# Kernel tuning notes

Measured on AMD Instinct MI355X. Metric: run time of the kernel, lower is better.

Reference implementation:

```python
import jax, jax.numpy as jnp
import numpy as np
from jax import lax

N, D, BATCH = 8192, 256, 64


def setup_inputs() -> dict:
    key = jax.random.key(0)
    V = jax.random.normal(key, (N, D), dtype=jnp.float32)
    V = V / jnp.linalg.norm(V, axis=1, keepdims=True)  # cosine = raw dot product
    return {
        "V": V,
        "cos_threshold": jnp.array([0.25], dtype=jnp.float32),
        "batch_size": BATCH,
    }


def reference(V, cos_threshold, batch_size):
    """Faithful port of Embeddings._fast_predict: batched cosine-sim thresholding
    followed by a sequential transitive merge of group ids.

    Returns group_ids [N] int32 (the clustering result; the torch code wraps this
    into a Matcher object, which is pure python bookkeeping).
    """
    n, d = V.shape
    B = int(batch_size)
    n_batches = n // B
    thr = cos_threshold[0]
    j_idx = jnp.arange(n, dtype=jnp.int32)
    group_init = jnp.arange(n, dtype=jnp.int32)

    def outer(gids, batch_start):
        # group ids as of the start of this batch (torch computes batch_matched
        # with these, but reads live group_ids inside the row loop via views)
        g0 = gids
        Vb = lax.dynamic_slice(V, (batch_start, 0), (B, d))        # [B, D]
        sims = Vb @ V.T                                            # [B, N]
        g0_i = lax.dynamic_slice(g0, (batch_start,), (B,))         # [B]
        jmask = j_idx > batch_start                                # j_slice = batch_start+1 .. N
        mask = (sims >= thr) & jmask[None, :] & (g0_i[:, None] != g0[None, :])  # [B, N]

        def inner(g, inp):
            k, row = inp
            gi = g[batch_start + k]  # live group id of row i (torch g_i is a view)
            # isin(group_ids, matched_groups): flag[label]=1 if any matched j has
            # current group label == label, then gather back through g
            flag = jnp.zeros(n, jnp.int32).at[g].max(row.astype(jnp.int32))
            g = jnp.where(flag[g] > 0, gi, g)
            return g, None

        gids, _ = lax.scan(inner, gids, (jnp.arange(B, dtype=jnp.int32), mask))
        return gids, None

    starts = jnp.arange(n_batches, dtype=jnp.int32) * B
    gids, _ = lax.scan(outer, group_init, starts)
    return gids
```

## Files before the change

kernel.cpp:

```cpp
#include <hip/hip_runtime.h>
#include <stdint.h>

#define NPTS 8192
#define DIM  256
#define CAP  32768
#define LDSE 8192
#define IBCAP 256
#define BAND 2.0e-3f

typedef _Float16 f16x8  __attribute__((ext_vector_type(8)));
typedef float    f32x16 __attribute__((ext_vector_type(16)));


__global__ __launch_bounds__(256) void convert_kernel(
        const float* __restrict__ V, _Float16* __restrict__ Vh,
        unsigned* __restrict__ ctr) {
    if (blockIdx.x == 0 && threadIdx.x == 0) { ctr[0] = 0u; ctr[1] = 0u; }
    size_t t = (size_t)blockIdx.x * 256 + threadIdx.x;
    const float4* src = reinterpret_cast<const float4*>(V) + t * 2;
    float4 v0 = src[0], v1 = src[1];
    f16x8 h;
    h[0] = (_Float16)v0.x; h[1] = (_Float16)v0.y;
    h[2] = (_Float16)v0.z; h[3] = (_Float16)v0.w;
    h[4] = (_Float16)v1.x; h[5] = (_Float16)v1.y;
    h[6] = (_Float16)v1.z; h[7] = (_Float16)v1.w;
    *reinterpret_cast<f16x8*>(Vh + t * 8) = h;
}

__global__ void init_count(unsigned* ctr) {
    if (threadIdx.x == 0) { ctr[0] = 0u; ctr[1] = 0u; }
}

__device__ __forceinline__ void gload_lds16(const void* g, void* l) {
    __builtin_amdgcn_global_load_lds(
        (const __attribute__((address_space(1))) void*)g,
        (__attribute__((address_space(3))) void*)l, 16, 0, 0);
}

__global__ __launch_bounds__(256, 2) void edge_mfma(
        const _Float16* __restrict__ Vh,
        const float* __restrict__ V,
        const float* __restrict__ thr_p,
        unsigned* __restrict__ ctr,
        unsigned* __restrict__ edges) {
    int t = blockIdx.x;
    int bi = (int)((65.0f - sqrtf(4225.0f - 4.0f * (float)t)) * 0.5f);
    if (bi > 31) bi = 31;
    while (bi > 0 && bi * (65 - bi) > t) --bi;
    while ((bi + 1) * (64 - bi) <= t) ++bi;
    int bj = 2 * bi + (t - bi * (65 - bi));

    __shared__ _Float16 LA[2][256 * 32];
    __shared__ _Float16 LB[2][128 * 32];
    __shared__ unsigned ibl[IBCAP];
    __shared__ unsigned ibn;

    const float thr = thr_p[0];
    const float hi = thr + BAND, lo = thr - BAND;
    const int tid  = threadIdx.x;
    const int lane = tid & 63;
    const int wid  = tid >> 6;
    const int wr = wid >> 1, wc = wid & 1;
    const int i0 = bi * 256, j0 = bj * 128;

    if (tid == 0) ibn = 0u;

    f32x16 acc[4][2];
#pragma unroll
    for (int a = 0; a < 4; ++a)
#pragma unroll
        for (int b = 0; b < 2; ++b) acc[a][b] = 0.0f;

    const int l31 = lane & 31, g = lane >> 5;
    const int srow = lane >> 2;
    const int sblk = lane & 3;

    auto STAGE = [&](int buf, int kc) {
#pragma unroll
        for (int q = 0; q < 6; ++q) {
            const int qq = wid * 6 + q;
            if (qq < 16) {
                const int grow = i0 + qq * 16 + srow;
                gload_lds16(Vh + ((size_t)grow * DIM + kc + sblk * 8),
                            &LA[buf][qq * 512]);
            } else {
                const int ins = qq - 16;
                const int grow = j0 + ins * 16 + srow;
                gload_lds16(Vh + ((size_t)grow * DIM + kc + sblk * 8),
                            &LB[buf][ins * 512]);
            }
        }
    };

    auto COMPUTE = [&](int buf) {
#pragma unroll
        for (int s = 0; s < 2; ++s) {
            const int xo = s * 16 + g * 8;
            f16x8 af[4], bf[2];
#pragma unroll
            for (int a = 0; a < 4; ++a)
                af[a] = *(const f16x8*)&LA[buf][(wr * 128 + a * 32 + l31) * 32 + xo];
#pragma unroll
            for (int b = 0; b < 2; ++b)
                bf[b] = *(const f16x8*)&LB[buf][(wc * 64 + b * 32 + l31) * 32 + xo];
#pragma unroll
            for (int a = 0; a < 4; ++a)
#pragma unroll
                for (int b = 0; b < 2; ++b)
                    acc[a][b] = __builtin_amdgcn_mfma_f32_32x32x16_f16(
                        af[a], bf[b], acc[a][b], 0, 0, 0);
        }
    };

    STAGE(0, 0);
    __syncthreads();
#pragma unroll
    for (int it = 0; it < 8; ++it) {
        if (it < 7) STAGE((it + 1) & 1, (it + 1) * 32);
        COMPUTE(it & 1);
        __syncthreads();
    }

#pragma unroll
    for (int a = 0; a < 4; ++a)
#pragma unroll
        for (int b = 0; b < 2; ++b)
#pragma unroll
            for (int reg = 0; reg < 16; ++reg) {
                float sim = acc[a][b][reg];
                int rr = (reg & 3) + 8 * (reg >> 2) + 4 * g;
                int i = i0 + wr * 128 + a * 32 + rr;
                int j = j0 + wc * 64 + b * 32 + l31;
                if (j > i && sim >= lo) {
                    unsigned key = ((unsigned)i << 13) | (unsigned)j;
                    if (sim >= hi) {
                        unsigned p = atomicAdd(&ctr[0], 1u);
                        if (p < CAP) edges[p] = key;
                    } else {
                        unsigned p = atomicAdd(&ibn, 1u);
                        if (p < IBCAP) ibl[p] = key;
                    }
                }
            }
    __syncthreads();

    unsigned nib = ibn; if (nib > IBCAP) nib = IBCAP;
    const double thrd = (double)thr;
    for (unsigned q = tid; q < nib; q += 256) {
        unsigned key = ibl[q];
        int i = (int)(key >> 13), j = (int)(key & 8191u);
        const float4* a4 = reinterpret_cast<const float4*>(V + (size_t)i * DIM);
        const float4* b4 = reinterpret_cast<const float4*>(V + (size_t)j * DIM);
        double s = 0.0;
#pragma unroll 4
        for (int k = 0; k < DIM / 4; ++k) {
            float4 x = a4[k], y = b4[k];
            s += (double)x.x * y.x + (double)x.y * y.y
               + (double)x.z * y.z + (double)x.w * y.w;
        }
        if (s >= thrd) {
            unsigned p = atomicAdd(&ctr[0], 1u);
            if (p < CAP) edges[p] = key;
        }
    }
}

__global__ __launch_bounds__(256) void edge_kernel(
        const float* __restrict__ V,
        const float* __restrict__ thr_p,
        unsigned*    __restrict__ ctr,
        unsigned*    __restrict__ edges) {
    const int bi = blockIdx.y, bj = blockIdx.x;
    if (bj < bi) return;

    __shared__ float As[128 * 32];
    __shared__ float Bs[128 * 32];

    const float thr = thr_p[0];
    const int tid = threadIdx.x;
    const int tx = tid & 15, ty = tid >> 4;
    const int i0 = bi * 128, j0 = bj * 128;

    float acc[8][8];
#pragma unroll
    for (int r = 0; r < 8; ++r)
#pragma unroll
        for (int c = 0; c < 8; ++c) acc[r][c] = 0.f;

    const int srow = tid >> 3, sq = tid & 7;

    for (int kc = 0; kc < DIM; kc += 32) {
#pragma unroll
        for (int p = 0; p < 4; ++p) {
            int row = srow + 32 * p;
            float4 va = *reinterpret_cast<const float4*>(
                &V[(size_t)(i0 + row) * DIM + kc + sq * 4]);
            float4 vb = *reinterpret_cast<const float4*>(
                &V[(size_t)(j0 + row) * DIM + kc + sq * 4]);
            int w = row * 32 + ((sq ^ ((row >> 3) & 7)) << 2);
            *reinterpret_cast<float4*>(&As[w]) = va;
            *reinterpret_cast<float4*>(&Bs[w]) = vb;
        }
        __syncthreads();
#pragma unroll
        for (int k4 = 0; k4 < 8; ++k4) {
            const float* pA = &As[(ty * 8) * 32 + ((k4 ^ (ty & 7)) << 2)];
            const float* pB = &Bs[(tx * 8) * 32 + ((k4 ^ (tx & 7)) << 2)];
            float4 a[8], b[8];
#pragma unroll
            for (int r = 0; r < 8; ++r)
                a[r] = *reinterpret_cast<const float4*>(&pA[r * 32]);
#pragma unroll
            for (int c = 0; c < 8; ++c)
                b[c] = *reinterpret_cast<const float4*>(&pB[c * 32]);
#pragma unroll
            for (int r = 0; r < 8; ++r)
#pragma unroll
                for (int c = 0; c < 8; ++c) {
                    acc[r][c] = fmaf(a[r].x, b[c].x, acc[r][c]);
                    acc[r][c] = fmaf(a[r].y, b[c].y, acc[r][c]);
                    acc[r][c] = fmaf(a[r].z, b[c].z, acc[r][c]);
                    acc[r][c] = fmaf(a[r].w, b[c].w, acc[r][c]);
                }
        }
        __syncthreads();
    }
#pragma unroll
    for (int r = 0; r < 8; ++r)
#pragma unroll
        for (int c = 0; c < 8; ++c) {
            int i = i0 + ty * 8 + r;
            int j = j0 + tx * 8 + c;
            if (j > i && acc[r][c] >= thr) {
                unsigned p = atomicAdd(&ctr[0], 1u);
                if (p < CAP) edges[p] = ((unsigned)i << 13) | (unsigned)j;
            }
        }
}

__global__ __launch_bounds__(1024) void uf_kernel(
        const unsigned* __restrict__ ctr,
        const unsigned* __restrict__ edges,
        int* __restrict__ out) {
    __shared__ int      par[NPTS];
    __shared__ unsigned slotA[NPTS];
    __shared__ unsigned slotB[NPTS];
    __shared__ unsigned sedge[LDSE];

    const int tid = threadIdx.x;

    unsigned EC = ctr[0]; if (EC > LDSE) EC = LDSE;

    for (int t = tid; t < NPTS; t += 1024) {
        par[t] = t; slotA[t] = 0xFFFFFFFFu; slotB[t] = 0xFFFFFFFFu;
    }
    for (unsigned e = tid; e < EC; e += 1024) sedge[e] = edges[e];
    __syncthreads();

    volatile int* vpar = par;

    for (int round = 0;; ++round) {
        unsigned* S = (round & 1) ? slotB : slotA;
        unsigned* T = (round & 1) ? slotA : slotB;

        for (unsigned e = tid; e < EC; e += 1024) {
            unsigned key = sedge[e];
            if (key & 0x80000000u) continue;
            int ri = (int)(key >> 13), rj = (int)(key & 8191u);
            int p;
            while ((p = vpar[ri]) != ri) ri = p;
            while ((p = vpar[rj]) != rj) rj = p;
            atomicMin(&S[ri], key);
            atomicMin(&S[rj], key);
        }
        __syncthreads();

        int mylive = 0;
        for (unsigned e = tid; e < EC; e += 1024) {
            unsigned key = sedge[e];
            if (key & 0x80000000u) continue;
            int i = (int)(key >> 13), j = (int)(key & 8191u);
            int ri = i, rj = j, p;
            while ((p = vpar[ri]) != ri) ri = p;
            while ((p = vpar[rj]) != rj) rj = p;
            if (S[ri] == key && S[rj] == key) {
                if (ri != rj) { par[rj] = ri; par[i] = ri; par[j] = ri; }
                sedge[e] = key | 0x80000000u;
            } else {
                mylive = 1;
            }
        }
        for (int t = tid; t < NPTS; t += 1024) T[t] = 0xFFFFFFFFu;
        if (__syncthreads_count(mylive) == 0) break;
    }

    for (int t = tid; t < NPTS; t += 1024) {
        int r = t, p;
        while ((p = par[r]) != r) r = p;
        out[t] = r;
    }
}

extern "C" void kernel_launch(void* const* d_in, const int* in_sizes, int n_in,
                              void* d_out, int out_size, void* d_ws, size_t ws_size,
                              hipStream_t stream) {
    const float* V     = (const float*)d_in[0];
    const float* thr_p = (const float*)d_in[1];

    unsigned* ctr   = (unsigned*)d_ws;
    unsigned* edges = (unsigned*)((char*)d_ws + 64);
    int*      out   = (int*)d_out;

    const size_t vhOff = 1u << 20;
    const size_t vN    = (size_t)NPTS * DIM;
    const size_t need  = vhOff + vN * sizeof(_Float16) + 65536;

    if (ws_size >= need) {
        _Float16* Vh = (_Float16*)((char*)d_ws + vhOff);
        hipLaunchKernelGGL(convert_kernel, dim3(1024), dim3(256), 0, stream,
                           V, Vh, ctr);
        hipLaunchKernelGGL(edge_mfma, dim3(1056), dim3(256), 0, stream,
                           Vh, V, thr_p, ctr, edges);
    } else {
        hipLaunchKernelGGL(init_count, dim3(1), dim3(64), 0, stream, ctr);
        hipLaunchKernelGGL(edge_kernel, dim3(64, 64), dim3(256), 0, stream,
                           V, thr_p, ctr, edges);
    }
    hipLaunchKernelGGL(uf_kernel, dim3(1), dim3(1024), 0, stream,
                       ctr, edges, out);
}
```

Baseline: 103.7 us.

## Triple-buffer LDS staging with explicit vmcnt waits and XOR swizzle

Moves the MFMA GEMM tile loop from double to triple buffering, so two k-chunks stay in flight. Explicit s_waitcnt vmcnt counts plus raw barriers replace __syncthreads, letting loads overlap compute. It also XOR-swizzles the LDS layout, via permuted lanes in the async global-to-LDS loads and a matching xor on fragment reads, to cut bank conflicts. This raises LDS use, which may lower occupancy at 2 blocks/CU, and relies on hand-counted vmcnt values being correct.

```diff
diff --git a/kernel.cpp b/kernel.cpp
--- a/kernel.cpp
+++ b/kernel.cpp
@@ -50,8 +50,8 @@
     while ((bi + 1) * (64 - bi) <= t) ++bi;
     int bj = 2 * bi + (t - bi * (65 - bi));
 
-    __shared__ _Float16 LA[2][256 * 32];
-    __shared__ _Float16 LB[2][128 * 32];
+    __shared__ _Float16 LA[3][256 * 32];
+    __shared__ _Float16 LB[3][128 * 32];
     __shared__ unsigned ibl[IBCAP];
     __shared__ unsigned ibn;
 
@@ -72,21 +72,23 @@
         for (int b = 0; b < 2; ++b) acc[a][b] = 0.0f;
 
     const int l31 = lane & 31, g = lane >> 5;
-    const int srow = lane >> 2;
-    const int sblk = lane & 3;
+    const int xl8 = (l31 & 7) << 3;
+    const int sl   = (lane ^ ((lane >> 2) & 7) ^ ((lane >> 4) & 1)) & 63;
+    const int lrow = sl >> 2;
+    const int lblk = sl & 3;
 
     auto STAGE = [&](int buf, int kc) {
 #pragma unroll
         for (int q = 0; q < 6; ++q) {
             const int qq = wid * 6 + q;
             if (qq < 16) {
-                const int grow = i0 + qq * 16 + srow;
-                gload_lds16(Vh + ((size_t)grow * DIM + kc + sblk * 8),
+                const int grow = i0 + qq * 16 + lrow;
+                gload_lds16(Vh + ((size_t)grow * DIM + kc + lblk * 8),
                             &LA[buf][qq * 512]);
             } else {
                 const int ins = qq - 16;
-                const int grow = j0 + ins * 16 + srow;
-                gload_lds16(Vh + ((size_t)grow * DIM + kc + sblk * 8),
+                const int grow = j0 + ins * 16 + lrow;
+                gload_lds16(Vh + ((size_t)grow * DIM + kc + lblk * 8),
                             &LB[buf][ins * 512]);
             }
         }
@@ -95,14 +97,18 @@
     auto COMPUTE = [&](int buf) {
 #pragma unroll
         for (int s = 0; s < 2; ++s) {
-            const int xo = s * 16 + g * 8;
+            const int xo = (2 * s + g) * 8;
             f16x8 af[4], bf[2];
 #pragma unroll
-            for (int a = 0; a < 4; ++a)
-                af[a] = *(const f16x8*)&LA[buf][(wr * 128 + a * 32 + l31) * 32 + xo];
-#pragma unroll
-            for (int b = 0; b < 2; ++b)
-                bf[b] = *(const f16x8*)&LB[buf][(wc * 64 + b * 32 + l31) * 32 + xo];
+            for (int a = 0; a < 4; ++a) {
+                const int row = wr * 128 + a * 32 + l31;
+                af[a] = *(const f16x8*)&LA[buf][(row * 32 + xo) ^ xl8];
+            }
+#pragma unroll
+            for (int b = 0; b < 2; ++b) {
+                const int row = wc * 64 + b * 32 + l31;
+                bf[b] = *(const f16x8*)&LB[buf][(row * 32 + xo) ^ xl8];
+            }
 #pragma unroll
             for (int a = 0; a < 4; ++a)
 #pragma unroll
@@ -113,12 +119,16 @@
     };
 
     STAGE(0, 0);
-    __syncthreads();
+    STAGE(1, 32);
 #pragma unroll
     for (int it = 0; it < 8; ++it) {
-        if (it < 7) STAGE((it + 1) & 1, (it + 1) * 32);
-        COMPUTE(it & 1);
-        __syncthreads();
+        if (it < 6) STAGE((it + 2) % 3, (it + 2) * 32);
+        if (it < 6)      asm volatile("s_waitcnt vmcnt(12)" ::: "memory");
+        else if (it == 6) asm volatile("s_waitcnt vmcnt(6)" ::: "memory");
+        else              asm volatile("s_waitcnt vmcnt(0)" ::: "memory");
+        __builtin_amdgcn_s_barrier();
+        COMPUTE(it % 3);
+        __builtin_amdgcn_s_barrier();
     }
 
 #pragma unroll
```

New measurement: 105.7 us. 2.0% more time.
